# Kernel optimization log

Hardware: AMD Instinct MI355X
Metric: run time of the kernel (lower is better)

Reference implementation:

```python
import jax, jax.numpy as jnp
import numpy as np

N_NODES = 100000
N_EDGES = 1600000
IN_CH = 128
HIDDEN = 128
OUT_CH = 64


def _glorot(key, shape):
    fan_in, fan_out = shape
    lim = jnp.sqrt(6.0 / (fan_in + fan_out))
    return jax.random.uniform(key, shape, jnp.float32, -lim, lim)


def setup_inputs() -> dict:
    key = jax.random.key(0)
    ks = jax.random.split(key, 8)
    x = jax.random.normal(ks[0], (N_NODES, IN_CH), jnp.float32)
    edge_index = jax.random.randint(ks[1], (2, N_EDGES), 0, N_NODES, jnp.int64)
    return {
        "x": x,
        "edge_index": edge_index,
        "W1": _glorot(ks[2], (IN_CH, HIDDEN)),
        "b1": jnp.zeros((HIDDEN,), jnp.float32),
        "W2": _glorot(ks[3], (HIDDEN, HIDDEN)),
        "b2": jnp.zeros((HIDDEN,), jnp.float32),
        "W3": _glorot(ks[4], (HIDDEN, HIDDEN)),
        "b3": jnp.zeros((HIDDEN,), jnp.float32),
        "Wout": _glorot(ks[5], (HIDDEN, OUT_CH)),
        "bout": jnp.zeros((OUT_CH,), jnp.float32),
    }


def _gcn_conv(h, W, b, src, dst, norm, num_nodes):
    # h: [N, F_in] -> linear transform first (PyG GCNConv order)
    h = h @ W                                   # [N, F_out]
    msg = h[src] * norm[:, None]                # [E+N, F_out] gathered+scaled
    agg = jax.ops.segment_sum(msg, dst, num_segments=num_nodes)
    return agg + b


def reference(x, edge_index, W1, b1, W2, b2, W3, b3, Wout, bout):
    n = x.shape[0]
    # add self-loops (PyG GCNConv default)
    loop = jnp.arange(n, dtype=edge_index.dtype)
    src = jnp.concatenate([edge_index[0], loop])
    dst = jnp.concatenate([edge_index[1], loop])
    # symmetric normalization: deg^-1/2[src] * deg^-1/2[dst]
    deg = jax.ops.segment_sum(jnp.ones_like(dst, dtype=x.dtype), dst, num_segments=n)
    inv_sqrt = jnp.where(deg > 0, jax.lax.rsqrt(deg), 0.0)
    norm = inv_sqrt[src] * inv_sqrt[dst]        # [E+N]

    h = jax.nn.relu(_gcn_conv(x, W1, b1, src, dst, norm, n))
    # dropout p=0.2 is identity in eval mode
    h = jax.nn.relu(_gcn_conv(h, W2, b2, src, dst, norm, n))
    h = _gcn_conv(h, W3, b3, src, dst, norm, n)
    return h @ Wout + bout                      # [N, OUT_CH]
```

## Files before the change

kernel.cpp:

```cpp
#include <hip/hip_runtime.h>

typedef unsigned int uint;
typedef _Float16 half_t;
typedef __attribute__((ext_vector_type(8))) _Float16 halfx8;
typedef __attribute__((ext_vector_type(4))) float floatx4;
typedef __attribute__((ext_vector_type(2))) int intx2;

constexpr int BSHIFT  = 9;
constexpr int BNODES  = 1 << BSHIFT;
constexpr int BCAP    = 9216;
constexpr int CSTRIDE = 16;
constexpr int CHUNK   = 8192;
constexpr int MAXBUK  = 256;

__global__ void k_zero(int* bcnt, int B) {
    int i = blockIdx.x * 256 + threadIdx.x;
    if (i < B) bcnt[i * CSTRIDE] = 0;
}

__global__ __launch_bounds__(256) void k_sortA(const int* __restrict__ ei,
                                               int* __restrict__ bcnt,
                                               uint* __restrict__ tmp, int E) {
    __shared__ uint ent[CHUNK];
    __shared__ unsigned char bid[CHUNK];
    __shared__ int hist[MAXBUK], lbase[MAXBUK], lcur[MAXBUK], gpos[MAXBUK];
    __shared__ int wsum[4];
    const int t = threadIdx.x;
    const int base = blockIdx.x * CHUNK;
    const int m = min(CHUNK, E - base);

    hist[t] = 0;
    __syncthreads();
    for (int i = t; i < m; i += 256)
        atomicAdd(&hist[ei[E + base + i] >> BSHIFT], 1);
    __syncthreads();
    {
        int lane = t & 63, w = t >> 6;
        int v = hist[t];
        int incl = v;
        for (int dd = 1; dd < 64; dd <<= 1) { int x = __shfl_up(incl, dd); if (lane >= dd) incl += x; }
        if (lane == 63) wsum[w] = incl;
        __syncthreads();
        int off = 0;
        for (int i = 0; i < w; i++) off += wsum[i];
        int excl = off + incl - v;
        lbase[t] = excl;
        lcur[t]  = excl;
        gpos[t]  = (v > 0) ? atomicAdd(&bcnt[t * CSTRIDE], v) : 0;
    }
    __syncthreads();
    for (int i = t; i < m; i += 256) {
        int s = ei[base + i];
        int d = ei[E + base + i];
        int b = d >> BSHIFT;
        int pos = atomicAdd(&lcur[b], 1);
        ent[pos] = (uint)s | ((uint)(d & (BNODES - 1)) << 17);
        bid[pos] = (unsigned char)b;
    }
    __syncthreads();
    for (int i = t; i < m; i += 256) {
        int b = bid[i];
        int g = gpos[b] + (i - lbase[b]);
        if (g < BCAP) tmp[(size_t)b * BCAP + g] = ent[i];
    }
}

__global__ void k_bucketScan(const int* __restrict__ bcnt, int* __restrict__ bbase,
                             int* __restrict__ row_ptr, int B, int N) {
    __shared__ int wsum[4];
    int t = threadIdx.x, lane = t & 63, w = t >> 6;
    int v = (t < B) ? min(bcnt[t * CSTRIDE], BCAP) : 0;
    int incl = v;
    for (int d = 1; d < 64; d <<= 1) { int x = __shfl_up(incl, d); if (lane >= d) incl += x; }
    if (lane == 63) wsum[w] = incl;
    __syncthreads();
    int off = 0;
    for (int i = 0; i < w; i++) off += wsum[i];
    int excl = off + incl - v;
    if (t <= B) bbase[t] = excl;
    if (t == B) row_ptr[N] = excl;
}

__global__ __launch_bounds__(256) void k_B1(const uint* __restrict__ tmp,
                                            const int* __restrict__ bcnt,
                                            const int* __restrict__ bbase,
                                            float* __restrict__ inv,
                                            int* __restrict__ row_ptr,
                                            int* __restrict__ rec_src, int N) {
    __shared__ int cnt[BNODES], cur[BNODES], pre[BNODES];
    __shared__ int wsum2[4];
    int b = blockIdx.x, t = threadIdx.x;
    int base = bbase[b], nbase = b << BSHIFT;
    cnt[t] = 0; cnt[t + 256] = 0;
    __syncthreads();
    int m = min(bcnt[b * CSTRIDE], BCAP);
    const uint* tp = tmp + (size_t)b * BCAP;
    for (int i = t; i < m; i += 256) atomicAdd(&cnt[tp[i] >> 17], 1);
    __syncthreads();
    int lane = t & 63, w = t >> 6;
    int c0 = cnt[2 * t], c1 = cnt[2 * t + 1];
    int v = c0 + c1;
    int incl = v;
    for (int dd = 1; dd < 64; dd <<= 1) { int x = __shfl_up(incl, dd); if (lane >= dd) incl += x; }
    if (lane == 63) wsum2[w] = incl;
    __syncthreads();
    int off = 0;
    for (int i = 0; i < w; i++) off += wsum2[i];
    int excl = off + incl - v;
    pre[2 * t] = excl;        pre[2 * t + 1] = excl + c0;
    cur[2 * t] = excl;        cur[2 * t + 1] = excl + c0;
    int n0 = nbase + 2 * t, n1 = nbase + 2 * t + 1;
    if (n0 < N) { inv[n0] = rsqrtf((float)(c0 + 1)); row_ptr[n0] = base + pre[2 * t]; }
    if (n1 < N) { inv[n1] = rsqrtf((float)(c1 + 1)); row_ptr[n1] = base + pre[2 * t + 1]; }
    __syncthreads();
    for (int i = t; i < m; i += 256) {
        uint wv = tp[i];
        int dlo = wv >> 17, s = (int)(wv & 0x1FFFFu);
        int pos = atomicAdd(&cur[dlo], 1);
        rec_src[base + pos] = s;
    }
}

__global__ __launch_bounds__(256) void k_B2(const int* __restrict__ rec_src,
                                            const int* __restrict__ row_ptr,
                                            const float* __restrict__ inv,
                                            const int* __restrict__ bbase,
                                            intx2* __restrict__ rec, int N) {
    __shared__ int rp[BNODES + 1];
    __shared__ float invd[BNODES];
    int b = blockIdx.x, t = threadIdx.x;
    int nbase = b << BSHIFT;
    int nn = min(BNODES, N - nbase);
    int base = bbase[b], endp = bbase[b + 1];
    for (int i = t; i < nn; i += 256) { rp[i] = row_ptr[nbase + i]; invd[i] = inv[nbase + i]; }
    if (t == 0) rp[nn] = endp;
    __syncthreads();
    for (int p = base + t; p < endp; p += 256) {
        int s = rec_src[p];
        int lo = 0, hi = nn;
        while (hi - lo > 1) { int mid = (lo + hi) >> 1; if (rp[mid] <= p) lo = mid; else hi = mid; }
        intx2 r; r[0] = s; r[1] = __float_as_int(inv[s] * invd[lo]);
        rec[p] = r;
    }
}

__global__ void k_compose(const float* __restrict__ W3, const float* __restrict__ Wout,
                          const float* __restrict__ b3, const float* __restrict__ bout,
                          float* __restrict__ Wc, float* __restrict__ bc) {
    int idx = blockIdx.x * 256 + threadIdx.x;
    if (idx < 128 * 64) {
        int i = idx >> 6, j = idx & 63;
        float s = 0.0f;
        for (int k = 0; k < 128; k++) s += W3[i * 128 + k] * Wout[k * 64 + j];
        Wc[idx] = s;
    } else if (idx < 128 * 64 + 64) {
        int j = idx - 128 * 64;
        float s = bout[j];
        for (int k = 0; k < 128; k++) s += b3[k] * Wout[k * 64 + j];
        bc[j] = s;
    }
}

__global__ void k_prepw(const float* __restrict__ W, half_t* __restrict__ Wh,
                        half_t* __restrict__ Wl, int K, int Nn) {
    int i = blockIdx.x * 256 + threadIdx.x;
    if (i < K * Nn) {
        int k = i / Nn, n = i % Nn;
        float w = W[(size_t)k * Nn + n];
        half_t h = (half_t)w;
        Wh[(size_t)n * K + k] = h;
        Wl[(size_t)n * K + k] = (half_t)(w - (float)h);
    }
}

template <typename AT, int NOUT>
__global__ __launch_bounds__(256) void k_gemm(const AT* __restrict__ A,
                                              const half_t* __restrict__ Wh,
                                              const half_t* __restrict__ Wl,
                                              half_t* __restrict__ Out, int nRows) {
    constexpr int CT = NOUT / 16;
    __shared__ __align__(16) half_t lds[NOUT * 136];

    const int tid = threadIdx.x;
    for (int i = tid; i < NOUT * 16; i += 256) {
        int r = i >> 4, c = i & 15;
        *(halfx8*)&lds[r * 136 + c * 8] = *(const halfx8*)&Wh[(size_t)r * 128 + c * 8];
    }
    __syncthreads();

    const int w = tid >> 6, lane = tid & 63;
    const int q = lane >> 4, m = lane & 15;
    const int rowBase = blockIdx.x * 128 + w * 32;
    int arow[2];
#pragma unroll
    for (int rt = 0; rt < 2; ++rt) {
        int r = rowBase + rt * 16 + m;
        arow[rt] = (r < nRows) ? r : (nRows - 1);
    }

    floatx4 acc[2][CT];
#pragma unroll
    for (int rt = 0; rt < 2; ++rt)
#pragma unroll
        for (int ct = 0; ct < CT; ++ct) acc[rt][ct] = (floatx4)0.0f;

    halfx8 a[2][4];
#pragma unroll
    for (int kk = 0; kk < 4; ++kk) {
#pragma unroll
        for (int rt = 0; rt < 2; ++rt) {
            const AT* ap = A + (size_t)arow[rt] * 128 + kk * 32 + q * 8;
            if constexpr (sizeof(AT) == 4) {
                floatx4 f0 = *(const floatx4*)ap;
                floatx4 f1 = *(const floatx4*)(ap + 4);
#pragma unroll
                for (int i = 0; i < 4; i++) { a[rt][kk][i] = (half_t)f0[i]; a[rt][kk][4 + i] = (half_t)f1[i]; }
            } else {
                a[rt][kk] = *(const halfx8*)ap;
            }
        }
#pragma unroll
        for (int ct = 0; ct < CT; ++ct) {
            halfx8 bh = *(const halfx8*)&lds[(ct * 16 + m) * 136 + kk * 32 + q * 8];
#pragma unroll
            for (int rt = 0; rt < 2; ++rt)
                acc[rt][ct] = __builtin_amdgcn_mfma_f32_16x16x32_f16(a[rt][kk], bh, acc[rt][ct], 0, 0, 0);
        }
    }
    __syncthreads();
    for (int i = tid; i < NOUT * 16; i += 256) {
        int r = i >> 4, c = i & 15;
        *(halfx8*)&lds[r * 136 + c * 8] = *(const halfx8*)&Wl[(size_t)r * 128 + c * 8];
    }
    __syncthreads();
#pragma unroll
    for (int kk = 0; kk < 4; ++kk)
#pragma unroll
        for (int ct = 0; ct < CT; ++ct) {
            halfx8 bl = *(const halfx8*)&lds[(ct * 16 + m) * 136 + kk * 32 + q * 8];
#pragma unroll
            for (int rt = 0; rt < 2; ++rt)
                acc[rt][ct] = __builtin_amdgcn_mfma_f32_16x16x32_f16(a[rt][kk], bl, acc[rt][ct], 0, 0, 0);
        }

#pragma unroll
    for (int rt = 0; rt < 2; ++rt)
#pragma unroll
        for (int ct = 0; ct < CT; ++ct) {
            int col = ct * 16 + m;
#pragma unroll
            for (int r = 0; r < 4; ++r) {
                int orow = rowBase + rt * 16 + q * 4 + r;
                if (orow < nRows)
                    Out[(size_t)orow * NOUT + col] = (half_t)acc[rt][ct][r];
            }
        }
}

template <int CH, typename OT, bool RELU>
__global__ __launch_bounds__(256) void k_agg(const half_t* __restrict__ tb,
                                             const intx2* __restrict__ rec,
                                             const int* __restrict__ row_ptr,
                                             const float* __restrict__ inv,
                                             const float* __restrict__ bias,
                                             OT* __restrict__ out, int N) {
    constexpr int L = CH / 8;
    constexpr int G = 64 / L;
    int wid = threadIdx.x >> 6, lane = threadIdx.x & 63;
    int d = blockIdx.x * 4 + wid;
    if (d >= N) return;
    int beg = row_ptr[d], end = row_ptr[d + 1];
    int grp = lane / L;
    int choff = (lane % L) * 8;
    float isd = inv[d];
    float ws0 = (grp == 0) ? isd * isd : 0.0f;

    halfx8 pself = *(const halfx8*)(tb + (size_t)d * CH + choff);
    float af[8];
#pragma unroll
    for (int c = 0; c < 8; c++) af[c] = ws0 * (float)pself[c];

    for (int e0 = beg; e0 < end; e0 += 64) {
        int me = e0 + lane;
        int sl = 0; float wl = 0.0f;
        if (me < end) { intx2 r = rec[me]; sl = r[0]; wl = __int_as_float(r[1]); }
        int cnt = end - e0; if (cnt > 64) cnt = 64;
        for (int j = 0; j < cnt; j += 4 * G) {
            int s4[4]; float w4[4];
#pragma unroll
            for (int u = 0; u < 4; u++) {
                int idx = j + u * G + grp;
                s4[u] = __shfl(sl, idx);
                w4[u] = __shfl(wl, idx);
            }
            halfx8 pv[4];
#pragma unroll
            for (int u = 0; u < 4; u++)
                pv[u] = *(const halfx8*)(tb + (size_t)s4[u] * CH + choff);
#pragma unroll
            for (int u = 0; u < 4; u++)
#pragma unroll
                for (int c = 0; c < 8; c++)
                    af[c] += w4[u] * (float)pv[u][c];
        }
    }
#pragma unroll
    for (int msk = L; msk < 64; msk <<= 1)
#pragma unroll
        for (int c = 0; c < 8; c++)
            af[c] += __shfl_xor(af[c], msk);

    if (lane < L) {
        int ch = lane * 8;
        floatx4 b0 = *(const floatx4*)(bias + ch);
        floatx4 b1 = *(const floatx4*)(bias + ch + 4);
#pragma unroll
        for (int c = 0; c < 8; c++) {
            af[c] += (c < 4) ? b0[c] : b1[c - 4];
            if (RELU) af[c] = fmaxf(af[c], 0.0f);
        }
        if constexpr (sizeof(OT) == 2) {
            halfx8 o;
#pragma unroll
            for (int c = 0; c < 8; c++) o[c] = (half_t)af[c];
            *(halfx8*)((half_t*)out + (size_t)d * CH + ch) = o;
        } else {
            floatx4 o0, o1;
#pragma unroll
            for (int c = 0; c < 4; c++) { o0[c] = af[c]; o1[c] = af[c + 4]; }
            *(floatx4*)((float*)out + (size_t)d * CH + ch) = o0;
            *(floatx4*)((float*)out + (size_t)d * CH + ch + 4) = o1;
        }
    }
}

extern "C" void kernel_launch(void* const* d_in, const int* in_sizes, int n_in,
                              void* d_out, int out_size, void* d_ws, size_t ws_size,
                              hipStream_t stream) {
    const int N = in_sizes[0] / 128;
    const int E = in_sizes[1] / 2;
    const int B = (N + BNODES - 1) >> BSHIFT;

    const float* x    = (const float*)d_in[0];
    const int*   ei   = (const int*)d_in[1];
    const float* W1   = (const float*)d_in[2];
    const float* b1   = (const float*)d_in[3];
    const float* W2   = (const float*)d_in[4];
    const float* b2   = (const float*)d_in[5];
    const float* W3   = (const float*)d_in[6];
    const float* b3   = (const float*)d_in[7];
    const float* Wout = (const float*)d_in[8];
    const float* bout = (const float*)d_in[9];
    float* out = (float*)d_out;

    char* p = (char*)d_ws;
    auto alloc = [&](size_t bytes) -> void* {
        void* r = (void*)p;
        p += (bytes + 255) & ~(size_t)255;
        return r;
    };
    int*    bcnt    = (int*)alloc((size_t)B * CSTRIDE * 4);
    int*    bbase   = (int*)alloc(((size_t)B + 1) * 4);
    uint*   tmp     = (uint*)alloc((size_t)B * BCAP * 4);
    int*    rec_src = (int*)alloc((size_t)E * 4);
    int*    row_ptr = (int*)alloc(((size_t)N + 1) * 4);
    float*  inv     = (float*)alloc((size_t)N * 4);
    intx2*  rec     = (intx2*)alloc((size_t)E * 8);
    float*  Wc      = (float*)alloc(128 * 64 * 4);
    float*  bc      = (float*)alloc(64 * 4);
    half_t* Wh1     = (half_t*)alloc(128 * 128 * 2);
    half_t* Wl1     = (half_t*)alloc(128 * 128 * 2);
    half_t* Wh2     = (half_t*)alloc(128 * 128 * 2);
    half_t* Wl2     = (half_t*)alloc(128 * 128 * 2);
    half_t* Whc     = (half_t*)alloc(64 * 128 * 2);
    half_t* Wlc     = (half_t*)alloc(64 * 128 * 2);
    half_t* hb      = (half_t*)alloc((size_t)N * 128 * 2);
    half_t* tb      = (half_t*)alloc((size_t)N * 128 * 2);

    const int gA = (E + CHUNK - 1) / CHUNK;
    const int gGemm = (N + 127) / 128;
    const int gAgg = (N + 3) / 4;

    k_zero<<<(B + 255) / 256, 256, 0, stream>>>(bcnt, B);
    k_sortA<<<gA, 256, 0, stream>>>(ei, bcnt, tmp, E);
    k_bucketScan<<<1, 256, 0, stream>>>(bcnt, bbase, row_ptr, B, N);
    k_B1<<<B, 256, 0, stream>>>(tmp, bcnt, bbase, inv, row_ptr, rec_src, N);
    k_B2<<<B, 256, 0, stream>>>(rec_src, row_ptr, inv, bbase, rec, N);

    k_compose<<<33, 256, 0, stream>>>(W3, Wout, b3, bout, Wc, bc);
    k_prepw<<<64, 256, 0, stream>>>(W1, Wh1, Wl1, 128, 128);
    k_prepw<<<64, 256, 0, stream>>>(W2, Wh2, Wl2, 128, 128);
    k_prepw<<<32, 256, 0, stream>>>(Wc, Whc, Wlc, 128, 64);

    k_gemm<float, 128><<<gGemm, 256, 0, stream>>>(x, Wh1, Wl1, tb, N);
    k_agg<128, half_t, true><<<gAgg, 256, 0, stream>>>(tb, rec, row_ptr, inv, b1, hb, N);
    k_gemm<half_t, 128><<<gGemm, 256, 0, stream>>>(hb, Wh2, Wl2, tb, N);
    k_agg<128, half_t, true><<<gAgg, 256, 0, stream>>>(tb, rec, row_ptr, inv, b2, hb, N);
    k_gemm<half_t, 64><<<gGemm, 256, 0, stream>>>(hb, Whc, Wlc, tb, N);
    k_agg<64, float, false><<<gAgg, 256, 0, stream>>>(tb, rec, row_ptr, inv, bc, out, N);
}
```

Baseline: 423.6 us.

## Merge preprocessing kernels into one launch, drop edge-weight array, widen gather unroll

Sort phase A, the first-layer GEMM (converting W1 to hi/lo fp16 inline), the W2 prep and the W3·Wout composition all run as branches of one kernel, so independent work overlaps and launches are cut. The B2 pass that built per-edge (src, weight) records is removed. Aggregation now reads only the source index and computes the weight as inv[src]*inv[dst] on the fly, which halves the edge-stream bytes but adds a dependent gather into inv. The aggregation inner loop issues 8 row loads per step instead of 4 for more memory-level parallelism, at some register cost.

```diff
diff --git a/kernel.cpp b/kernel.cpp
--- a/kernel.cpp
+++ b/kernel.cpp
@@ -4,7 +4,6 @@
 typedef _Float16 half_t;
 typedef __attribute__((ext_vector_type(8))) _Float16 halfx8;
 typedef __attribute__((ext_vector_type(4))) float floatx4;
-typedef __attribute__((ext_vector_type(2))) int intx2;
 
 constexpr int BSHIFT  = 9;
 constexpr int BNODES  = 1 << BSHIFT;
@@ -13,55 +12,158 @@
 constexpr int CHUNK   = 8192;
 constexpr int MAXBUK  = 256;
 
-__global__ void k_zero(int* bcnt, int B) {
-    int i = blockIdx.x * 256 + threadIdx.x;
-    if (i < B) bcnt[i * CSTRIDE] = 0;
-}
-
-__global__ __launch_bounds__(256) void k_sortA(const int* __restrict__ ei,
-                                               int* __restrict__ bcnt,
-                                               uint* __restrict__ tmp, int E) {
-    __shared__ uint ent[CHUNK];
-    __shared__ unsigned char bid[CHUNK];
-    __shared__ int hist[MAXBUK], lbase[MAXBUK], lcur[MAXBUK], gpos[MAXBUK];
-    __shared__ int wsum[4];
-    const int t = threadIdx.x;
-    const int base = blockIdx.x * CHUNK;
-    const int m = min(CHUNK, E - base);
-
-    hist[t] = 0;
-    __syncthreads();
-    for (int i = t; i < m; i += 256)
-        atomicAdd(&hist[ei[E + base + i] >> BSHIFT], 1);
-    __syncthreads();
-    {
-        int lane = t & 63, w = t >> 6;
-        int v = hist[t];
-        int incl = v;
-        for (int dd = 1; dd < 64; dd <<= 1) { int x = __shfl_up(incl, dd); if (lane >= dd) incl += x; }
-        if (lane == 63) wsum[w] = incl;
-        __syncthreads();
-        int off = 0;
-        for (int i = 0; i < w; i++) off += wsum[i];
-        int excl = off + incl - v;
-        lbase[t] = excl;
-        lcur[t]  = excl;
-        gpos[t]  = (v > 0) ? atomicAdd(&bcnt[t * CSTRIDE], v) : 0;
-    }
-    __syncthreads();
-    for (int i = t; i < m; i += 256) {
-        int s = ei[base + i];
-        int d = ei[E + base + i];
-        int b = d >> BSHIFT;
-        int pos = atomicAdd(&lcur[b], 1);
-        ent[pos] = (uint)s | ((uint)(d & (BNODES - 1)) << 17);
-        bid[pos] = (unsigned char)b;
-    }
-    __syncthreads();
-    for (int i = t; i < m; i += 256) {
-        int b = bid[i];
-        int g = gpos[b] + (i - lbase[b]);
-        if (g < BCAP) tmp[(size_t)b * BCAP + g] = ent[i];
+__global__ __launch_bounds__(256) void k_mega0(
+    const float* __restrict__ x, const int* __restrict__ ei,
+    const float* __restrict__ W1, const float* __restrict__ W2,
+    const float* __restrict__ W3, const float* __restrict__ Wout,
+    const float* __restrict__ b3, const float* __restrict__ bout,
+    int* __restrict__ bcnt, uint* __restrict__ tmp, half_t* __restrict__ tb,
+    half_t* __restrict__ Wh2, half_t* __restrict__ Wl2,
+    half_t* __restrict__ Whc, half_t* __restrict__ Wlc, float* __restrict__ bc,
+    int N, int E, int nSort, int nGemm) {
+    __shared__ __align__(16) char smem[45088];
+    const int bx = blockIdx.x, t = threadIdx.x;
+
+    if (bx < nSort) {
+        uint* ent = (uint*)smem;
+        unsigned char* bid = (unsigned char*)(smem + 32768);
+        int* hist  = (int*)(smem + 40960);
+        int* lbase = hist + 256;
+        int* lcur  = hist + 512;
+        int* gpos  = hist + 768;
+        int* wsum  = hist + 1024;
+        const int base = bx * CHUNK;
+        const int m = min(CHUNK, E - base);
+        hist[t] = 0;
+        __syncthreads();
+        for (int i = t; i < m; i += 256)
+            atomicAdd(&hist[ei[E + base + i] >> BSHIFT], 1);
+        __syncthreads();
+        {
+            int lane = t & 63, w = t >> 6;
+            int v = hist[t];
+            int incl = v;
+            for (int dd = 1; dd < 64; dd <<= 1) { int xsh = __shfl_up(incl, dd); if (lane >= dd) incl += xsh; }
+            if (lane == 63) wsum[w] = incl;
+            __syncthreads();
+            int off = 0;
+            for (int i = 0; i < w; i++) off += wsum[i];
+            int excl = off + incl - v;
+            lbase[t] = excl;
+            lcur[t]  = excl;
+            gpos[t]  = (v > 0) ? atomicAdd(&bcnt[t * CSTRIDE], v) : 0;
+        }
+        __syncthreads();
+        for (int i = t; i < m; i += 256) {
+            int s = ei[base + i];
+            int d = ei[E + base + i];
+            int b = d >> BSHIFT;
+            int pos = atomicAdd(&lcur[b], 1);
+            ent[pos] = (uint)s | ((uint)(d & (BNODES - 1)) << 17);
+            bid[pos] = (unsigned char)b;
+        }
+        __syncthreads();
+        for (int i = t; i < m; i += 256) {
+            int b = bid[i];
+            int g = gpos[b] + (i - lbase[b]);
+            if (g < BCAP) tmp[(size_t)b * BCAP + g] = ent[i];
+        }
+    } else if (bx < nSort + nGemm) {
+        half_t* ldsW = (half_t*)smem;
+        const int gb = bx - nSort;
+        for (int i = t; i < 128 * 32; i += 256) {
+            int k = i >> 5, n4 = (i & 31) << 2;
+            floatx4 w4 = *(const floatx4*)&W1[k * 128 + n4];
+#pragma unroll
+            for (int u = 0; u < 4; u++) ldsW[(n4 + u) * 136 + k] = (half_t)w4[u];
+        }
+        __syncthreads();
+        const int w = t >> 6, lane = t & 63;
+        const int q = lane >> 4, mm = lane & 15;
+        const int rowBase = gb * 128 + w * 32;
+        int arow[2];
+#pragma unroll
+        for (int rt = 0; rt < 2; ++rt) {
+            int r = rowBase + rt * 16 + mm;
+            arow[rt] = (r < N) ? r : (N - 1);
+        }
+        floatx4 acc[2][8];
+#pragma unroll
+        for (int rt = 0; rt < 2; ++rt)
+#pragma unroll
+            for (int ct = 0; ct < 8; ++ct) acc[rt][ct] = (floatx4)0.0f;
+        halfx8 a[2][4];
+#pragma unroll
+        for (int kk = 0; kk < 4; ++kk) {
+#pragma unroll
+            for (int rt = 0; rt < 2; ++rt) {
+                const float* ap = x + (size_t)arow[rt] * 128 + kk * 32 + q * 8;
+                floatx4 f0 = *(const floatx4*)ap;
+                floatx4 f1 = *(const floatx4*)(ap + 4);
+#pragma unroll
+                for (int i = 0; i < 4; i++) { a[rt][kk][i] = (half_t)f0[i]; a[rt][kk][4 + i] = (half_t)f1[i]; }
+            }
+#pragma unroll
+            for (int ct = 0; ct < 8; ++ct) {
+                halfx8 bh = *(const halfx8*)&ldsW[(ct * 16 + mm) * 136 + kk * 32 + q * 8];
+#pragma unroll
+                for (int rt = 0; rt < 2; ++rt)
+                    acc[rt][ct] = __builtin_amdgcn_mfma_f32_16x16x32_f16(a[rt][kk], bh, acc[rt][ct], 0, 0, 0);
+            }
+        }
+        __syncthreads();
+        for (int i = t; i < 128 * 32; i += 256) {
+            int k = i >> 5, n4 = (i & 31) << 2;
+            floatx4 w4 = *(const floatx4*)&W1[k * 128 + n4];
+#pragma unroll
+            for (int u = 0; u < 4; u++) {
+                half_t h = (half_t)w4[u];
+                ldsW[(n4 + u) * 136 + k] = (half_t)(w4[u] - (float)h);
+            }
+        }
+        __syncthreads();
+#pragma unroll
+        for (int kk = 0; kk < 4; ++kk)
+#pragma unroll
+            for (int ct = 0; ct < 8; ++ct) {
+                halfx8 bl = *(const halfx8*)&ldsW[(ct * 16 + mm) * 136 + kk * 32 + q * 8];
+#pragma unroll
+                for (int rt = 0; rt < 2; ++rt)
+                    acc[rt][ct] = __builtin_amdgcn_mfma_f32_16x16x32_f16(a[rt][kk], bl, acc[rt][ct], 0, 0, 0);
+            }
+#pragma unroll
+        for (int rt = 0; rt < 2; ++rt)
+#pragma unroll
+            for (int ct = 0; ct < 8; ++ct) {
+                int col = ct * 16 + mm;
+#pragma unroll
+                for (int r = 0; r < 4; ++r) {
+                    int orow = rowBase + rt * 16 + q * 4 + r;
+                    if (orow < N) tb[(size_t)orow * 128 + col] = (half_t)acc[rt][ct][r];
+                }
+            }
+    } else if (bx < nSort + nGemm + 64) {
+        int i = (bx - nSort - nGemm) * 256 + t;
+        int k = i >> 7, n = i & 127;
+        float wv = W2[k * 128 + n];
+        half_t h = (half_t)wv;
+        Wh2[n * 128 + k] = h;
+        Wl2[n * 128 + k] = (half_t)(wv - (float)h);
+    } else {
+        int i = (bx - nSort - nGemm - 64) * 256 + t;
+        if (i < 128 * 64) {
+            int r = i >> 6, j = i & 63;
+            float s = 0.0f;
+            for (int k = 0; k < 128; k++) s += W3[r * 128 + k] * Wout[k * 64 + j];
+            half_t h = (half_t)s;
+            Whc[j * 128 + r] = h;
+            Wlc[j * 128 + r] = (half_t)(s - (float)h);
+        } else if (i < 128 * 64 + 64) {
+            int j = i - 128 * 64;
+            float s = bout[j];
+            for (int k = 0; k < 128; k++) s += b3[k] * Wout[k * 64 + j];
+            bc[j] = s;
+        }
     }
 }
 
@@ -86,8 +188,8 @@
                                             const int* __restrict__ bbase,
                                             float* __restrict__ inv,
                                             int* __restrict__ row_ptr,
-                                            int* __restrict__ rec_src, int N) {
-    __shared__ int cnt[BNODES], cur[BNODES], pre[BNODES];
+                                            int* __restrict__ colv, int N) {
+    __shared__ int cnt[BNODES], cur[BNODES];
     __shared__ int wsum2[4];
     int b = blockIdx.x, t = threadIdx.x;
     int base = bbase[b], nbase = b << BSHIFT;
@@ -107,87 +209,33 @@
     int off = 0;
     for (int i = 0; i < w; i++) off += wsum2[i];
     int excl = off + incl - v;
-    pre[2 * t] = excl;        pre[2 * t + 1] = excl + c0;
-    cur[2 * t] = excl;        cur[2 * t + 1] = excl + c0;
     int n0 = nbase + 2 * t, n1 = nbase + 2 * t + 1;
-    if (n0 < N) { inv[n0] = rsqrtf((float)(c0 + 1)); row_ptr[n0] = base + pre[2 * t]; }
-    if (n1 < N) { inv[n1] = rsqrtf((float)(c1 + 1)); row_ptr[n1] = base + pre[2 * t + 1]; }
+    __syncthreads();
+    cur[2 * t] = excl; cur[2 * t + 1] = excl + c0;
+    if (n0 < N) { inv[n0] = rsqrtf((float)(c0 + 1)); row_ptr[n0] = base + excl; }
+    if (n1 < N) { inv[n1] = rsqrtf((float)(c1 + 1)); row_ptr[n1] = base + excl + c0; }
     __syncthreads();
     for (int i = t; i < m; i += 256) {
         uint wv = tp[i];
         int dlo = wv >> 17, s = (int)(wv & 0x1FFFFu);
         int pos = atomicAdd(&cur[dlo], 1);
-        rec_src[base + pos] = s;
-    }
-}
-
-__global__ __launch_bounds__(256) void k_B2(const int* __restrict__ rec_src,
-                                            const int* __restrict__ row_ptr,
-                                            const float* __restrict__ inv,
-                                            const int* __restrict__ bbase,
-                                            intx2* __restrict__ rec, int N) {
-    __shared__ int rp[BNODES + 1];
-    __shared__ float invd[BNODES];
-    int b = blockIdx.x, t = threadIdx.x;
-    int nbase = b << BSHIFT;
-    int nn = min(BNODES, N - nbase);
-    int base = bbase[b], endp = bbase[b + 1];
-    for (int i = t; i < nn; i += 256) { rp[i] = row_ptr[nbase + i]; invd[i] = inv[nbase + i]; }
-    if (t == 0) rp[nn] = endp;
-    __syncthreads();
-    for (int p = base + t; p < endp; p += 256) {
-        int s = rec_src[p];
-        int lo = 0, hi = nn;
-        while (hi - lo > 1) { int mid = (lo + hi) >> 1; if (rp[mid] <= p) lo = mid; else hi = mid; }
-        intx2 r; r[0] = s; r[1] = __float_as_int(inv[s] * invd[lo]);
-        rec[p] = r;
-    }
-}
-
-__global__ void k_compose(const float* __restrict__ W3, const float* __restrict__ Wout,
-                          const float* __restrict__ b3, const float* __restrict__ bout,
-                          float* __restrict__ Wc, float* __restrict__ bc) {
-    int idx = blockIdx.x * 256 + threadIdx.x;
-    if (idx < 128 * 64) {
-        int i = idx >> 6, j = idx & 63;
-        float s = 0.0f;
-        for (int k = 0; k < 128; k++) s += W3[i * 128 + k] * Wout[k * 64 + j];
-        Wc[idx] = s;
-    } else if (idx < 128 * 64 + 64) {
-        int j = idx - 128 * 64;
-        float s = bout[j];
-        for (int k = 0; k < 128; k++) s += b3[k] * Wout[k * 64 + j];
-        bc[j] = s;
-    }
-}
-
-__global__ void k_prepw(const float* __restrict__ W, half_t* __restrict__ Wh,
-                        half_t* __restrict__ Wl, int K, int Nn) {
-    int i = blockIdx.x * 256 + threadIdx.x;
-    if (i < K * Nn) {
-        int k = i / Nn, n = i % Nn;
-        float w = W[(size_t)k * Nn + n];
-        half_t h = (half_t)w;
-        Wh[(size_t)n * K + k] = h;
-        Wl[(size_t)n * K + k] = (half_t)(w - (float)h);
-    }
-}
-
-template <typename AT, int NOUT>
-__global__ __launch_bounds__(256) void k_gemm(const AT* __restrict__ A,
+        colv[base + pos] = s;
+    }
+}
+
+template <int NOUT>
+__global__ __launch_bounds__(256) void k_gemm(const half_t* __restrict__ A,
                                               const half_t* __restrict__ Wh,
                                               const half_t* __restrict__ Wl,
                                               half_t* __restrict__ Out, int nRows) {
     constexpr int CT = NOUT / 16;
     __shared__ __align__(16) half_t lds[NOUT * 136];
-
     const int tid = threadIdx.x;
     for (int i = tid; i < NOUT * 16; i += 256) {
         int r = i >> 4, c = i & 15;
         *(halfx8*)&lds[r * 136 + c * 8] = *(const halfx8*)&Wh[(size_t)r * 128 + c * 8];
     }
     __syncthreads();
-
     const int w = tid >> 6, lane = tid & 63;
     const int q = lane >> 4, m = lane & 15;
     const int rowBase = blockIdx.x * 128 + w * 32;
@@ -197,28 +245,17 @@
         int r = rowBase + rt * 16 + m;
         arow[rt] = (r < nRows) ? r : (nRows - 1);
     }
-
     floatx4 acc[2][CT];
 #pragma unroll
     for (int rt = 0; rt < 2; ++rt)
 #pragma unroll
         for (int ct = 0; ct < CT; ++ct) acc[rt][ct] = (floatx4)0.0f;
-
     halfx8 a[2][4];
 #pragma unroll
     for (int kk = 0; kk < 4; ++kk) {
 #pragma unroll
-        for (int rt = 0; rt < 2; ++rt) {
-            const AT* ap = A + (size_t)arow[rt] * 128 + kk * 32 + q * 8;
-            if constexpr (sizeof(AT) == 4) {
-                floatx4 f0 = *(const floatx4*)ap;
-                floatx4 f1 = *(const floatx4*)(ap + 4);
-#pragma unroll
-                for (int i = 0; i < 4; i++) { a[rt][kk][i] = (half_t)f0[i]; a[rt][kk][4 + i] = (half_t)f1[i]; }
-            } else {
-                a[rt][kk] = *(const halfx8*)ap;
-            }
-        }
+        for (int rt = 0; rt < 2; ++rt)
+            a[rt][kk] = *(const halfx8*)(A + (size_t)arow[rt] * 128 + kk * 32 + q * 8);
 #pragma unroll
         for (int ct = 0; ct < CT; ++ct) {
             halfx8 bh = *(const halfx8*)&lds[(ct * 16 + m) * 136 + kk * 32 + q * 8];
@@ -242,7 +279,6 @@
             for (int rt = 0; rt < 2; ++rt)
                 acc[rt][ct] = __builtin_amdgcn_mfma_f32_16x16x32_f16(a[rt][kk], bl, acc[rt][ct], 0, 0, 0);
         }
-
 #pragma unroll
     for (int rt = 0; rt < 2; ++rt)
 #pragma unroll
@@ -259,7 +295,7 @@
 
 template <int CH, typename OT, bool RELU>
 __global__ __launch_bounds__(256) void k_agg(const half_t* __restrict__ tb,
-                                             const intx2* __restrict__ rec,
+                                             const int* __restrict__ colv,
                                              const int* __restrict__ row_ptr,
                                              const float* __restrict__ inv,
                                              const float* __restrict__ bias,
@@ -283,25 +319,25 @@
     for (int e0 = beg; e0 < end; e0 += 64) {
         int me = e0 + lane;
         int sl = 0; float wl = 0.0f;
-        if (me < end) { intx2 r = rec[me]; sl = r[0]; wl = __int_as_float(r[1]); }
+        if (me < end) { sl = colv[me]; wl = inv[sl] * isd; }
         int cnt = end - e0; if (cnt > 64) cnt = 64;
-        for (int j = 0; j < cnt; j += 4 * G) {
-            int s4[4]; float w4[4];
-#pragma unroll
-            for (int u = 0; u < 4; u++) {
+        for (int j = 0; j < cnt; j += 8 * G) {
+            int s8[8]; float w8[8];
+#pragma unroll
+            for (int u = 0; u < 8; u++) {
                 int idx = j + u * G + grp;
-                s4[u] = __shfl(sl, idx);
-                w4[u] = __shfl(wl, idx);
-            }
-            halfx8 pv[4];
-#pragma unroll
-            for (int u = 0; u < 4; u++)
-                pv[u] = *(const halfx8*)(tb + (size_t)s4[u] * CH + choff);
-#pragma unroll
-            for (int u = 0; u < 4; u++)
+                s8[u] = __shfl(sl, idx);
+                w8[u] = __shfl(wl, idx);
+            }
+            halfx8 pv[8];
+#pragma unroll
+            for (int u = 0; u < 8; u++)
+                pv[u] = *(const halfx8*)(tb + (size_t)s8[u] * CH + choff);
+#pragma unroll
+            for (int u = 0; u < 8; u++)
 #pragma unroll
                 for (int c = 0; c < 8; c++)
-                    af[c] += w4[u] * (float)pv[u][c];
+                    af[c] += w8[u] * (float)pv[u][c];
         }
     }
 #pragma unroll
@@ -362,14 +398,10 @@
     int*    bcnt    = (int*)alloc((size_t)B * CSTRIDE * 4);
     int*    bbase   = (int*)alloc(((size_t)B + 1) * 4);
     uint*   tmp     = (uint*)alloc((size_t)B * BCAP * 4);
-    int*    rec_src = (int*)alloc((size_t)E * 4);
+    int*    colv    = (int*)alloc((size_t)E * 4);
     int*    row_ptr = (int*)alloc(((size_t)N + 1) * 4);
     float*  inv     = (float*)alloc((size_t)N * 4);
-    intx2*  rec     = (intx2*)alloc((size_t)E * 8);
-    float*  Wc      = (float*)alloc(128 * 64 * 4);
     float*  bc      = (float*)alloc(64 * 4);
-    half_t* Wh1     = (half_t*)alloc(128 * 128 * 2);
-    half_t* Wl1     = (half_t*)alloc(128 * 128 * 2);
     half_t* Wh2     = (half_t*)alloc(128 * 128 * 2);
     half_t* Wl2     = (half_t*)alloc(128 * 128 * 2);
     half_t* Whc     = (half_t*)alloc(64 * 128 * 2);
@@ -377,25 +409,21 @@
     half_t* hb      = (half_t*)alloc((size_t)N * 128 * 2);
     half_t* tb      = (half_t*)alloc((size_t)N * 128 * 2);
 
-    const int gA = (E + CHUNK - 1) / CHUNK;
-    const int gGemm = (N + 127) / 128;
-    const int gAgg = (N + 3) / 4;
-
-    k_zero<<<(B + 255) / 256, 256, 0, stream>>>(bcnt, B);
-    k_sortA<<<gA, 256, 0, stream>>>(ei, bcnt, tmp, E);
+    const int nSort = (E + CHUNK - 1) / CHUNK;
+    const int nGemm = (N + 127) / 128;
+    const int gMega = nSort + nGemm + 64 + 33;
+    const int gAgg  = (N + 3) / 4;
+
+    hipMemsetAsync(bcnt, 0, (size_t)B * CSTRIDE * 4, stream);
+    k_mega0<<<gMega, 256, 0, stream>>>(x, ei, W1, W2, W3, Wout, b3, bout,
+                                       bcnt, tmp, tb, Wh2, Wl2, Whc, Wlc, bc,
+                                       N, E, nSort, nGemm);
     k_bucketScan<<<1, 256, 0, stream>>>(bcnt, bbase, row_ptr, B, N);
-    k_B1<<<B, 256, 0, stream>>>(tmp, bcnt, bbase, inv, row_ptr, rec_src, N);
-    k_B2<<<B, 256, 0, stream>>>(rec_src, row_ptr, inv, bbase, rec, N);
-
-    k_compose<<<33, 256, 0, stream>>>(W3, Wout, b3, bout, Wc, bc);
-    k_prepw<<<64, 256, 0, stream>>>(W1, Wh1, Wl1, 128, 128);
-    k_prepw<<<64, 256, 0, stream>>>(W2, Wh2, Wl2, 128, 128);
-    k_prepw<<<32, 256, 0, stream>>>(Wc, Whc, Wlc, 128, 64);
-
-    k_gemm<float, 128><<<gGemm, 256, 0, stream>>>(x, Wh1, Wl1, tb, N);
-    k_agg<128, half_t, true><<<gAgg, 256, 0, stream>>>(tb, rec, row_ptr, inv, b1, hb, N);
-    k_gemm<half_t, 128><<<gGemm, 256, 0, stream>>>(hb, Wh2, Wl2, tb, N);
-    k_agg<128, half_t, true><<<gAgg, 256, 0, stream>>>(tb, rec, row_ptr, inv, b2, hb, N);
-    k_gemm<half_t, 64><<<gGemm, 256, 0, stream>>>(hb, Whc, Wlc, tb, N);
-    k_agg<64, float, false><<<gAgg, 256, 0, stream>>>(tb, rec, row_ptr, inv, bc, out, N);
-}
+    k_B1<<<B, 256, 0, stream>>>(tmp, bcnt, bbase, inv, row_ptr, colv, N);
+
+    k_agg<128, half_t, true><<<gAgg, 256, 0, stream>>>(tb, colv, row_ptr, inv, b1, hb, N);
+    k_gemm<128><<<nGemm, 256, 0, stream>>>(hb, Wh2, Wl2, tb, N);
+    k_agg<128, half_t, true><<<gAgg, 256, 0, stream>>>(tb, colv, row_ptr, inv, b2, hb, N);
+    k_gemm<64><<<nGemm, 256, 0, stream>>>(hb, Whc, Wlc, tb, N);
+    k_agg<64, float, false><<<gAgg, 256, 0, stream>>>(tb, colv, row_ptr, inv, bc, out, N);
+}
```

Result: no change. 428.5 us (+1.1%).
